# Optimization experiments

Hardware: AMD Instinct MI355X
Metric: run time of the kernel (lower is better)

The kernel has to match this reference:

```python
import jax, jax.numpy as jnp
import numpy as np
from jax import lax

TAU = 2.0          # spikingjelly LIFNode default tau
VTH = 1.0          # v_threshold
ALPHA = 2.0        # ATan surrogate alpha (grad only; fwd is heaviside)
N_WIN = (2, 4, 4)
TOPK = 4
HEADS = 8
EPS = 1e-5


@jax.custom_vjp
def spike(x):
    return (x >= 0).astype(x.dtype)

def _spike_fwd(x):
    return (x >= 0).astype(x.dtype), x

def _spike_bwd(x, g):
    sg = (ALPHA / 2.0) / (1.0 + (jnp.pi / 2.0 * ALPHA * x) ** 2)
    return (g * sg,)

spike.defvjp(_spike_fwd, _spike_bwd)


def lif(x_seq):
    # multi-step LIF, v_reset=None (soft reset), decay_input=True, detach_reset
    def step(v, x):
        v = v + (x - v) / TAU
        s = spike(v - VTH)
        v = v - lax.stop_gradient(s) * VTH
        return v, s
    v0 = jnp.zeros_like(x_seq[0])
    _, s_seq = lax.scan(step, v0, x_seq)
    return s_seq


def bn3d(x, g, b):
    # track_running_stats=False -> always batch stats; step_mode 'm' folds T into batch.
    # x: [T,B,C,Lt,Lh,Lw]; normalize per-channel over (T,B,Lt,Lh,Lw)
    ax = (0, 1, 3, 4, 5)
    m = x.mean(ax, keepdims=True)
    v = x.var(ax, keepdims=True)
    sh = (1, 1, -1, 1, 1, 1)
    return g.reshape(sh) * (x - m) * lax.rsqrt(v + EPS) + b.reshape(sh)


def bra(x, wqkv, bqkv, lepe_w, wo, bo):
    # Bi-level routing attention over 3D windows. x: [N, Lt, Lh, Lw, C]
    N, Lt, Lh, Lw, C = x.shape
    nt, nh, nw = N_WIN
    rt, rh, rw = Lt // nt, Lh // nh, Lw // nw
    R, P = nt * nh * nw, rt * rh * rw
    Dh = C // HEADS

    qkv = x @ wqkv + bqkv                       # [N,Lt,Lh,Lw,3C]
    q, k, v = jnp.split(qkv, 3, axis=-1)

    def to_reg(t):  # -> [N, R, P, C]
        t = t.reshape(N, nt, rt, nh, rh, nw, rw, C)
        return t.transpose(0, 1, 3, 5, 2, 4, 6, 7).reshape(N, R, P, C)

    def from_reg(t):  # [N,R,P,C] -> [N,Lt,Lh,Lw,C]
        t = t.reshape(N, nt, nh, nw, rt, rh, rw, C)
        return t.transpose(0, 1, 4, 2, 5, 3, 6, 7).reshape(N, Lt, Lh, Lw, C)

    qr, kr, vr = to_reg(q), to_reg(k), to_reg(v)

    # coarse routing: region means, top-k region selection
    a_r = jnp.einsum('nrc,nsc->nrs', qr.mean(2), kr.mean(2))   # [N,R,R]
    _, idx = lax.top_k(a_r, TOPK)                               # [N,R,TOPK]

    # gather selected regions' k,v: [N,R,TOPK,P,C] -> [N,R,TOPK*P,H,Dh]
    kg = jax.vmap(lambda a, i: a[i])(kr, idx)
    vg = jax.vmap(lambda a, i: a[i])(vr, idx)
    kg = kg.reshape(N, R, TOPK * P, HEADS, Dh)
    vg = vg.reshape(N, R, TOPK * P, HEADS, Dh)
    qh = qr.reshape(N, R, P, HEADS, Dh)

    logits = jnp.einsum('nrphd,nrkhd->nrhpk', qh * (Dh ** -0.5), kg)
    attn = jax.nn.softmax(logits, axis=-1)
    out = jnp.einsum('nrhpk,nrkhd->nrphd', attn, vg).reshape(N, R, P, C)
    out = from_reg(out)

    # LEPE: depthwise 3x3x3 conv on v
    v_ncdhw = v.transpose(0, 4, 1, 2, 3)
    lepe = lax.conv_general_dilated(
        v_ncdhw, lepe_w, (1, 1, 1), 'SAME', feature_group_count=C,
        dimension_numbers=('NCDHW', 'OIDHW', 'NCDHW'))
    out = out + lepe.transpose(0, 2, 3, 4, 1)

    return out @ wo + bo


def setup_inputs() -> dict:
    key = jax.random.key(0)
    ks = jax.random.split(key, 8)
    T, B, C, Lt, Lh, Lw = 2, 1, 256, 8, 32, 32
    inp = {
        'x': jax.random.normal(ks[0], (T, B, C, Lt, Lh, Lw), jnp.float32),
        'bn1_g': jnp.ones((C,), jnp.float32),
        'bn1_b': jnp.zeros((C,), jnp.float32),
        'wqkv': jax.random.normal(ks[1], (C, 3 * C), jnp.float32) * (C ** -0.5),
        'bqkv': jnp.zeros((3 * C,), jnp.float32),
        'lepe_w': jax.random.normal(ks[2], (C, 1, 3, 3, 3), jnp.float32) * 0.1,
        'wo': jax.random.normal(ks[3], (C, C), jnp.float32) * (C ** -0.5),
        'bo': jnp.zeros((C,), jnp.float32),
        'bn2_g': jnp.ones((C,), jnp.float32),
        'bn2_b': jnp.zeros((C,), jnp.float32),
        'ffn_w1': jax.random.normal(ks[4], (C, 4 * C), jnp.float32) * (C ** -0.5),
        'ffn_b1': jnp.zeros((4 * C,), jnp.float32),
        'ffn_w2': jax.random.normal(ks[5], (4 * C, C), jnp.float32) * ((4 * C) ** -0.5),
        'ffn_b2': jnp.zeros((C,), jnp.float32),
        'scale': jnp.ones((1,), jnp.float32) * 0.5,
    }
    return inp


def reference(x, bn1_g, bn1_b, wqkv, bqkv, lepe_w, wo, bo,
              bn2_g, bn2_b, ffn_w1, ffn_b1, ffn_w2, ffn_b2, scale):
    T, B, C, Lt, Lh, Lw = x.shape

    # --- attention branch ---
    s1 = lif(bn3d(x, bn1_g, bn1_b))                       # [T,B,C,Lt,Lh,Lw]
    sa = s1.transpose(0, 1, 3, 4, 5, 2).reshape(T * B, Lt, Lh, Lw, C)
    a = bra(sa, wqkv, bqkv, lepe_w, wo, bo)
    a = a.reshape(T, B, Lt, Lh, Lw, C).transpose(0, 1, 5, 2, 3, 4)
    x = x + a * scale

    # --- FFN branch (1x1x1 conv = channel GEMM) ---
    s2 = lif(bn3d(x, bn2_g, bn2_b))
    h = jax.nn.gelu(jnp.einsum('tbcdhw,cf->tbfdhw', s2, ffn_w1)
                    + ffn_b1.reshape(1, 1, -1, 1, 1, 1), approximate=False)
    f = (jnp.einsum('tbfdhw,fc->tbcdhw', h, ffn_w2)
         + ffn_b2.reshape(1, 1, -1, 1, 1, 1))
    return x + f * scale
```

## Files before the change

kernel.cpp:

```cpp
#include <hip/hip_runtime.h>
#include <math.h>

#define CC 256
#define LL 8192
#define RR 32
#define PPP 256
#define NTOP 4
#define TOKS 16384
#define TBLK (TOKS * 32)

typedef unsigned short u16;
typedef __attribute__((ext_vector_type(8))) short short8;
typedef __attribute__((ext_vector_type(8))) unsigned short u16x8;
typedef __attribute__((ext_vector_type(4))) float f32x4;
typedef __attribute__((ext_vector_type(4))) unsigned short u16x4;

#if defined(__has_builtin)
#if __has_builtin(__builtin_amdgcn_exp2f)
#define EXP2(x) __builtin_amdgcn_exp2f(x)
#endif
#endif
#ifndef EXP2
#define EXP2(x) exp2f(x)
#endif

__device__ inline u16 f2bf(float f) {
  unsigned int b = __float_as_uint(f);
  unsigned int r = (b + 0x7FFFu + ((b >> 16) & 1u)) >> 16;
  return (u16)r;
}
__device__ inline float bf2f(u16 x) { return __uint_as_float(((unsigned int)x) << 16); }

__global__ __launch_bounds__(256) void k_bnstats(const float* __restrict__ x,
                                                 float* __restrict__ mean,
                                                 float* __restrict__ istd) {
  int c = blockIdx.x, tid = threadIdx.x;
  float s = 0.f, sq = 0.f;
  for (int i = tid; i < 2 * LL / 4; i += 256) {
    int t = i >> 11, l4 = (i & 2047) * 4;
    float4 v = *(const float4*)&x[(size_t)(t * CC + c) * LL + l4];
    s += (v.x + v.y) + (v.z + v.w);
    sq += (v.x * v.x + v.y * v.y) + (v.z * v.z + v.w * v.w);
  }
  __shared__ float rs[256], rq[256];
  rs[tid] = s; rq[tid] = sq;
  __syncthreads();
  for (int off = 128; off > 0; off >>= 1) {
    if (tid < off) { rs[tid] += rs[tid + off]; rq[tid] += rq[tid + off]; }
    __syncthreads();
  }
  if (tid == 0) {
    float m = rs[0] * (1.f / (2 * LL));
    float var = rq[0] * (1.f / (2 * LL)) - m * m;
    mean[c] = m;
    istd[c] = rsqrtf(var + 1e-5f);
  }
}

__global__ __launch_bounds__(128) void k_bnfin(const float* __restrict__ psum,
                                               const float* __restrict__ psq,
                                               float* __restrict__ mean,
                                               float* __restrict__ istd) {
  int c = blockIdx.x;
  int tid = threadIdx.x;
  __shared__ float rs[128], rq[128];
  rs[tid] = psum[c * 128 + tid];
  rq[tid] = psq[c * 128 + tid];
  __syncthreads();
  for (int off = 64; off > 0; off >>= 1) {
    if (tid < off) { rs[tid] += rs[tid + off]; rq[tid] += rq[tid + off]; }
    __syncthreads();
  }
  if (tid == 0) {
    float m = rs[0] * (1.f / 16384.f);
    float var = rq[0] * (1.f / 16384.f) - m * m;
    mean[c] = m;
    istd[c] = rsqrtf(var + 1e-5f);
  }
}

__global__ __launch_bounds__(256) void k_lifT(const float* __restrict__ xin,
                                              const float* __restrict__ mean,
                                              const float* __restrict__ istd,
                                              const float* __restrict__ g,
                                              const float* __restrict__ b,
                                              u16* __restrict__ actT) {
  __shared__ float t0[32][33], t1[32][33];
  int l0 = blockIdx.x * 32, c0 = blockIdx.y * 32;
  int tx = threadIdx.x & 31, ty = threadIdx.x >> 5;
  for (int i = 0; i < 32; i += 8) {
    int c = c0 + ty + i;
    float m = mean[c], is = istd[c], gg = g[c], bb = b[c];
    float x0 = xin[(size_t)c * LL + l0 + tx];
    float x1 = xin[(size_t)(CC + c) * LL + l0 + tx];
    float y0 = gg * (x0 - m) * is + bb;
    float y1 = gg * (x1 - m) * is + bb;
    float v = y0 * 0.5f;
    float s0 = (v >= 1.f) ? 1.f : 0.f;
    v -= s0;
    v += (y1 - v) * 0.5f;
    float s1 = (v >= 1.f) ? 1.f : 0.f;
    t0[ty + i][tx] = s0;
    t1[ty + i][tx] = s1;
  }
  __syncthreads();
  size_t kb = (size_t)(c0 >> 5) * TBLK;
  for (int i = 0; i < 32; i += 8) {
    int l = l0 + ty + i;
    actT[kb + (size_t)l * 32 + tx] = f2bf(t0[tx][ty + i]);
    actT[kb + (size_t)(LL + l) * 32 + tx] = f2bf(t1[tx][ty + i]);
  }
}

__device__ inline void tr_tile(const float* __restrict__ in, u16* __restrict__ out,
                               int C, int c0, int r0) {
  __shared__ float t[32][33];
  int tx = threadIdx.x & 31, ty = threadIdx.x >> 5;
  for (int i = 0; i < 32; i += 8)
    t[ty + i][tx] = in[(size_t)(r0 + ty + i) * C + c0 + tx];
  __syncthreads();
  size_t kb = (size_t)(r0 >> 5) * C * 32;
  for (int i = 0; i < 32; i += 8)
    out[kb + (size_t)(c0 + ty + i) * 32 + tx] = f2bf(t[tx][ty + i]);
}

__global__ __launch_bounds__(256) void k_trall(const float* __restrict__ wqkv,
                                               const float* __restrict__ w1,
                                               const float* __restrict__ w2,
                                               const float* __restrict__ wo,
                                               const float* __restrict__ lep,
                                               u16* __restrict__ wqkvT, u16* __restrict__ w1T,
                                               u16* __restrict__ w2T, u16* __restrict__ woT,
                                               float* __restrict__ wTlep) {
  int b = blockIdx.x;
  if (b < 192) {
    tr_tile(wqkv, wqkvT, 768, (b % 24) * 32, (b / 24) * 32);
  } else if (b < 448) {
    int i = b - 192;
    tr_tile(w1, w1T, 1024, (i % 32) * 32, (i / 32) * 32);
  } else if (b < 704) {
    int i = b - 448;
    tr_tile(w2, w2T, 256, (i % 8) * 32, (i / 8) * 32);
  } else if (b < 768) {
    int i = b - 704;
    tr_tile(wo, woT, 256, (i % 8) * 32, (i / 8) * 32);
  } else {
    int c = threadIdx.x;
    for (int tap = 0; tap < 27; ++tap) wTlep[tap * 256 + c] = lep[c * 27 + tap];
  }
}

template<int MR, int NR, int WCN, int KTOT>
__device__ inline void mfma_core_blk(const u16* __restrict__ A0, int sAb,
                                     const u16* __restrict__ B0, int sBb,
                                     f32x4 acc[MR][NR]) {
  int lane = threadIdx.x & 63;
  int w = threadIdx.x >> 6;
  int wr = w / WCN, wc = w % WCN;
  int u = lane & 15;
  int g8 = (lane >> 4) * 8;
  const u16* Ap = A0 + (wr * MR * 16 + u) * 32 + g8;
  const u16* Bp = B0 + (wc * NR * 16 + u) * 32 + g8;
  constexpr int NKB = KTOT >> 5;
  short8 aA[MR], bA[NR], aB[MR], bB[NR];
#pragma unroll
  for (int i = 0; i < MR; ++i) aA[i] = *(const short8*)(Ap + i * 512);
#pragma unroll
  for (int j = 0; j < NR; ++j) bA[j] = *(const short8*)(Bp + j * 512);
#pragma unroll
  for (int kb = 0; kb < NKB; kb += 2) {
    if (kb + 1 < NKB) {
#pragma unroll
      for (int i = 0; i < MR; ++i) aB[i] = *(const short8*)(Ap + (size_t)(kb + 1) * sAb + i * 512);
#pragma unroll
      for (int j = 0; j < NR; ++j) bB[j] = *(const short8*)(Bp + (size_t)(kb + 1) * sBb + j * 512);
    }
#pragma unroll
    for (int i = 0; i < MR; ++i)
#pragma unroll
      for (int j = 0; j < NR; ++j)
        acc[i][j] = __builtin_amdgcn_mfma_f32_16x16x32_bf16(aA[i], bA[j], acc[i][j], 0, 0, 0);
    if (kb + 2 < NKB) {
#pragma unroll
      for (int i = 0; i < MR; ++i) aA[i] = *(const short8*)(Ap + (size_t)(kb + 2) * sAb + i * 512);
#pragma unroll
      for (int j = 0; j < NR; ++j) bA[j] = *(const short8*)(Bp + (size_t)(kb + 2) * sBb + j * 512);
    }
    if (kb + 1 < NKB) {
#pragma unroll
      for (int i = 0; i < MR; ++i)
#pragma unroll
        for (int j = 0; j < NR; ++j)
          acc[i][j] = __builtin_amdgcn_mfma_f32_16x16x32_bf16(aB[i], bB[j], acc[i][j], 0, 0, 0);
    }
  }
}

__global__ __launch_bounds__(256) void k_gqkv(const u16* __restrict__ spkT, const u16* __restrict__ wT,
                                              const float* __restrict__ bias,
                                              u16* __restrict__ qh, u16* __restrict__ kh,
                                              u16* __restrict__ vt, u16* __restrict__ vtok) {
  f32x4 acc[4][4] = {};
  int m0 = blockIdx.x * 128, n0 = blockIdx.y * 128;
  mfma_core_blk<4, 4, 2, 256>(spkT + (size_t)m0 * 32, TBLK, wT + (size_t)n0 * 32, 768 * 32, acc);
  int lane = threadIdx.x & 63, w = threadIdx.x >> 6;
  int wr = w >> 1, wc = w & 1;
  int u = lane & 15;
  const float QSC = 0.255034865f;
#pragma unroll
  for (int i = 0; i < 4; ++i) {
    int token0 = m0 + wr * 64 + i * 16 + (lane >> 4) * 4;
    int l = token0 & (LL - 1), nb = token0 >> 13;
    int lt = l >> 10, lh = (l >> 5) & 31, lw = l & 31;
    int r = ((lt >> 2) * 4 + (lh >> 3)) * 4 + (lw >> 3);
    int p0 = ((lt & 3) * 8 + (lh & 7)) * 8 + (lw & 7);
    int nr = nb * RR + r;
#pragma unroll
    for (int j = 0; j < 4; ++j) {
      int ch = n0 + wc * 64 + j * 16 + u;
      int which = ch >> 8, c = ch & 255;
      int hh = c >> 5, dh = c & 31;
      size_t hb = ((size_t)nr * 8 + hh) * 8192;
      float bb = bias[ch];
      if (which == 0) {
#pragma unroll
        for (int reg = 0; reg < 4; ++reg)
          qh[hb + (p0 + reg) * 32 + dh] = f2bf((acc[i][j][reg] + bb) * QSC);
      } else if (which == 1) {
#pragma unroll
        for (int reg = 0; reg < 4; ++reg)
          kh[hb + (p0 + reg) * 32 + dh] = f2bf(acc[i][j][reg] + bb);
      } else {
        u16x4 pk;
#pragma unroll
        for (int reg = 0; reg < 4; ++reg) {
          u16 vb = f2bf(acc[i][j][reg] + bb);
          pk[reg] = vb;
          vtok[(size_t)(token0 + reg) * CC + c] = vb;
        }
        *(u16x4*)&vt[hb + dh * 256 + p0] = pk;
      }
    }
  }
}

__global__ __launch_bounds__(256) void k_means(const u16* __restrict__ qh, const u16* __restrict__ kh,
                                               float* __restrict__ qm, float* __restrict__ km) {
  int nrh = blockIdx.x;
  int nr = nrh >> 3, h = nrh & 7;
  int tid = threadIdx.x;
  int dh = tid & 31, pg = tid >> 5;
  size_t base = (size_t)nrh * 8192;
  float sq = 0.f, sk = 0.f;
  for (int p = pg * 32; p < pg * 32 + 32; ++p) {
    sq += bf2f(qh[base + p * 32 + dh]);
    sk += bf2f(kh[base + p * 32 + dh]);
  }
  __shared__ float rq[256], rk[256];
  rq[tid] = sq; rk[tid] = sk;
  __syncthreads();
  if (pg == 0) {
#pragma unroll
    for (int g = 1; g < 8; ++g) { sq += rq[g * 32 + dh]; sk += rk[g * 32 + dh]; }
    qm[nr * 256 + h * 32 + dh] = sq * (1.f / 256);
    km[nr * 256 + h * 32 + dh] = sk * (1.f / 256);
  }
}

__global__ __launch_bounds__(256) void k_route(const float* __restrict__ qm,
                                               const float* __restrict__ km,
                                               int* __restrict__ idx) {
  int nr = blockIdx.x;
  int n = nr >> 5;
  int tid = threadIdx.x;
  int s = tid >> 3, cg = tid & 7;
  const float* qrow = qm + nr * CC;
  const float* krow = km + (n * RR + s) * CC;
  float sum = 0.f;
  for (int c = cg * 32; c < cg * 32 + 32; ++c) sum += qrow[c] * krow[c];
  sum += __shfl_xor(sum, 1);
  sum += __shfl_xor(sum, 2);
  sum += __shfl_xor(sum, 4);
  __shared__ float ar[32];
  if (cg == 0) ar[s] = sum;
  __syncthreads();
  if (tid == 0) {
    for (int t = 0; t < NTOP; ++t) {
      float best = -1e30f; int bi = 0;
      for (int ss = 0; ss < 32; ++ss)
        if (ar[ss] > best) { best = ar[ss]; bi = ss; }
      ar[bi] = -1e30f;
      idx[nr * NTOP + t] = bi;
    }
  }
}

__global__ __launch_bounds__(256) void k_attn_mfma(const u16* __restrict__ qh,
                                                   const u16* __restrict__ kh,
                                                   const u16* __restrict__ vt,
                                                   const int* __restrict__ idx,
                                                   u16* __restrict__ oreg) {
  int h = blockIdx.x, r = blockIdx.y, n = blockIdx.z;
  int nr = n * RR + r;
  int lane = threadIdx.x & 63;
  int w = threadIdx.x >> 6;
  int u = lane & 15, g = lane >> 4;
  int swz = (u >> 1) & 3;
  __shared__ __align__(16) unsigned pl[4096];
  unsigned* plw = &pl[w * 1024];

  const u16* qb = qh + ((size_t)nr * 8 + h) * 8192;
  int q0 = w * 64;
  short8 qf[4];
#pragma unroll
  for (int f = 0; f < 4; ++f)
    qf[f] = *(const short8*)(qb + (size_t)(q0 + f * 16 + u) * 32 + g * 8);

  f32x4 accO[2][4] = {};
  float lsum[4] = {0.f, 0.f, 0.f, 0.f};
  const int* idxp = &idx[nr * NTOP];

  for (int ri = 0; ri < NTOP; ++ri) {
    int reg = idxp[ri];
    size_t rb = ((size_t)(n * RR + reg) * 8 + h) * 8192;
#pragma unroll 2
    for (int t = 0; t < 8; ++t) {
      int pb = t * 32;
      short8 kf0 = *(const short8*)(kh + rb + (size_t)(pb + u) * 32 + g * 8);
      short8 kf1 = *(const short8*)(kh + rb + (size_t)(pb + 16 + u) * 32 + g * 8);
      short8 vf0 = *(const short8*)(vt + rb + (size_t)u * 256 + pb + g * 8);
      short8 vf1 = *(const short8*)(vt + rb + (size_t)(16 + u) * 256 + pb + g * 8);

      f32x4 s0[4], s1[4];
      __builtin_amdgcn_s_setprio(1);
#pragma unroll
      for (int nf = 0; nf < 4; ++nf) {
        s0[nf] = __builtin_amdgcn_mfma_f32_16x16x32_bf16(kf0, qf[nf], (f32x4){0.f, 0.f, 0.f, 0.f}, 0, 0, 0);
        s1[nf] = __builtin_amdgcn_mfma_f32_16x16x32_bf16(kf1, qf[nf], (f32x4){0.f, 0.f, 0.f, 0.f}, 0, 0, 0);
      }
      __builtin_amdgcn_s_setprio(0);
#pragma unroll
      for (int nf = 0; nf < 4; ++nf) {
#pragma unroll
        for (int mf = 0; mf < 2; ++mf) {
          f32x4 sv = mf ? s1[nf] : s0[nf];
          float p0 = EXP2(sv[0]);
          float p1 = EXP2(sv[1]);
          float p2 = EXP2(sv[2]);
          float p3 = EXP2(sv[3]);
          lsum[nf] += (p0 + p1) + (p2 + p3);
          unsigned wA, wB;
          asm("v_cvt_pk_bf16_f32 %0, %1, %2" : "=v"(wA) : "v"(p0), "v"(p1));
          asm("v_cvt_pk_bf16_f32 %0, %1, %2" : "=v"(wB) : "v"(p2), "v"(p3));
          int bidx = (mf * 2 + (g >> 1)) ^ swz;
          *(uint2*)&plw[nf * 256 + u * 16 + bidx * 4 + (g & 1) * 2] = make_uint2(wA, wB);
        }
      }
      __builtin_amdgcn_s_setprio(1);
#pragma unroll
      for (int nf = 0; nf < 4; ++nf) {
        short8 pf = *(const short8*)&plw[nf * 256 + u * 16 + ((g ^ swz) << 2)];
        accO[0][nf] = __builtin_amdgcn_mfma_f32_16x16x32_bf16(vf0, pf, accO[0][nf], 0, 0, 0);
        accO[1][nf] = __builtin_amdgcn_mfma_f32_16x16x32_bf16(vf1, pf, accO[1][nf], 0, 0, 0);
      }
      __builtin_amdgcn_s_setprio(0);
    }
  }

#pragma unroll
  for (int nf = 0; nf < 4; ++nf) {
    lsum[nf] += __shfl_xor(lsum[nf], 16);
    lsum[nf] += __shfl_xor(lsum[nf], 32);
    float inv = 1.f / lsum[nf];
    int q = q0 + nf * 16 + u;
    int z = (((r >> 4) & 1) << 2) | ((q >> 6) & 3);
    int y = (((r >> 2) & 3) << 3) | ((q >> 3) & 7);
    int xx = ((r & 3) << 3) | (q & 7);
    int l = (z << 10) | (y << 5) | xx;
    u16* ob = &oreg[((size_t)(n * LL + l)) * CC + h * 32];
#pragma unroll
    for (int mf = 0; mf < 2; ++mf) {
      f32x4 o = mf ? accO[1][nf] : accO[0][nf];
      float a0 = o[0] * inv, a1 = o[1] * inv, a2 = o[2] * inv, a3 = o[3] * inv;
      unsigned w0, w1;
      asm("v_cvt_pk_bf16_f32 %0, %1, %2" : "=v"(w0) : "v"(a0), "v"(a1));
      asm("v_cvt_pk_bf16_f32 %0, %1, %2" : "=v"(w1) : "v"(a2), "v"(a3));
      *(uint2*)&ob[mf * 16 + g * 4] = make_uint2(w0, w1);
    }
  }
}

__global__ __launch_bounds__(256) void k_lepe(const u16* __restrict__ oreg,
                                              const u16* __restrict__ vtok,
                                              const float* __restrict__ wT,
                                              u16* __restrict__ otok) {
  int vox = threadIdx.x >> 6;
  int b = blockIdx.x * 4 + vox;
  int l = b & (LL - 1);
  int lt = l >> 10, lh = (l >> 5) & 31, lw = l & 31;
  int c4 = (threadIdx.x & 63) * 4;
  const u16* vb = vtok + (size_t)b * CC + c4;
  float lx = 0.f, ly = 0.f, lz = 0.f, lww = 0.f;
#pragma unroll
  for (int dz = -1; dz <= 1; ++dz) {
#pragma unroll
    for (int dy = -1; dy <= 1; ++dy) {
#pragma unroll
      for (int dx = -1; dx <= 1; ++dx) {
        int z = lt + dz, y = lh + dy, xx = lw + dx;
        if (z >= 0 && z < 8 && y >= 0 && y < 32 && xx >= 0 && xx < 32) {
          int tap = ((dz + 1) * 3 + (dy + 1)) * 3 + (dx + 1);
          long off = (long)(dz * 1024 + dy * 32 + dx) * CC;
          float4 w4 = *(const float4*)&wT[tap * 256 + c4];
          u16x4 v4 = *(const u16x4*)&vb[off];
          lx = fmaf(w4.x, bf2f(v4[0]), lx);
          ly = fmaf(w4.y, bf2f(v4[1]), ly);
          lz = fmaf(w4.z, bf2f(v4[2]), lz);
          lww = fmaf(w4.w, bf2f(v4[3]), lww);
        }
      }
    }
  }
  u16x4 a4 = *(const u16x4*)&oreg[(size_t)b * CC + c4];
  size_t oaddr = (size_t)(c4 >> 5) * TBLK + (size_t)b * 32 + (c4 & 31);
  *(u16x4*)&otok[oaddr] =
      (u16x4){f2bf(bf2f(a4[0]) + lx), f2bf(bf2f(a4[1]) + ly),
              f2bf(bf2f(a4[2]) + lz), f2bf(bf2f(a4[3]) + lww)};
}

__global__ __launch_bounds__(256) void k_gffn1(const u16* __restrict__ sT, const u16* __restrict__ wT,
                                               const float* __restrict__ bias, u16* __restrict__ hbuf) {
  __shared__ __align__(16) u16 ot[4 * 128 * 40];
  f32x4 acc[4][4] = {};
  int m0 = blockIdx.x * 128, n0 = blockIdx.y * 128;
  mfma_core_blk<4, 4, 2, 256>(sT + (size_t)m0 * 32, TBLK, wT + (size_t)n0 * 32, 1024 * 32, acc);
  int lane = threadIdx.x & 63, w = threadIdx.x >> 6;
  int wr = w >> 1, wc = w & 1;
  int u = lane & 15, g = lane >> 4;
#pragma unroll
  for (int i = 0; i < 4; ++i) {
#pragma unroll
    for (int reg = 0; reg < 4; ++reg) {
      int tl = wr * 64 + i * 16 + g * 4 + reg;
#pragma unroll
      for (int j = 0; j < 4; ++j) {
        int cl = wc * 64 + j * 16 + u;
        float z = acc[i][j][reg] + bias[n0 + cl];
        float z2 = z * z;
        float ea = z * fmaf(z2, 0.1029431f, 2.3022078f);
        float t = EXP2(ea);
        float th = (t - 1.f) * __builtin_amdgcn_rcpf(t + 1.f);
        float hz = 0.5f * z;
        float gel = fmaf(hz, th, hz);
        ot[(cl >> 5) * (128 * 40) + tl * 40 + (cl & 31)] = f2bf(gel);
      }
    }
  }
  __syncthreads();
  int kb = threadIdx.x >> 6;
  int lt2 = threadIdx.x & 63;
  int tok0 = lt2 >> 2, chunk = lt2 & 3;
  u16* gdst = hbuf + ((size_t)(n0 >> 5) + kb) * TBLK + (size_t)m0 * 32;
  const u16* lsrc = &ot[kb * (128 * 40)];
#pragma unroll
  for (int it = 0; it < 8; ++it) {
    int token = it * 16 + tok0;
    *(u16x8*)(gdst + (size_t)token * 32 + chunk * 8) =
        *(const u16x8*)(lsrc + token * 40 + chunk * 8);
  }
}

__global__ __launch_bounds__(128) void k_gffn2(const u16* __restrict__ w2T, const u16* __restrict__ hb,
                                               const float* __restrict__ bias, const float* __restrict__ scale,
                                               float* __restrict__ out) {
  f32x4 acc[2][4] = {};
  int n0 = blockIdx.x * 128, m0 = blockIdx.y * 32;
  mfma_core_blk<2, 4, 2, 1024>(w2T + (size_t)m0 * 32, 256 * 32, hb + (size_t)n0 * 32, TBLK, acc);
  int lane = threadIdx.x & 63, wc = threadIdx.x >> 6;
  float sc = scale[0];
#pragma unroll
  for (int i = 0; i < 2; ++i) {
#pragma unroll
    for (int reg = 0; reg < 4; ++reg) {
      int ch = m0 + i * 16 + (lane >> 4) * 4 + reg;
      float bb = bias[ch];
#pragma unroll
      for (int j = 0; j < 4; ++j) {
        int token = n0 + wc * 64 + j * 16 + (lane & 15);
        int t = token >> 13, l = token & (LL - 1);
        size_t oi = ((size_t)t * CC + ch) * LL + l;
        out[oi] += (acc[i][j][reg] + bb) * sc;
      }
    }
  }
}

__global__ __launch_bounds__(128) void k_gwo(const u16* __restrict__ woT, const u16* __restrict__ atok,
                                             const float* __restrict__ bias, const float* __restrict__ xin,
                                             const float* __restrict__ scale, float* __restrict__ out,
                                             float* __restrict__ psum, float* __restrict__ psq) {
  f32x4 acc[2][4] = {};
  int n0 = blockIdx.x * 128, m0 = blockIdx.y * 32;
  mfma_core_blk<2, 4, 2, 256>(woT + (size_t)m0 * 32, 256 * 32, atok + (size_t)n0 * 32, TBLK, acc);
  int lane = threadIdx.x & 63, wc = threadIdx.x >> 6;
  int g = lane >> 4;
  float sc = scale[0];
  __shared__ float lsum[2][32], lsq[2][32];
#pragma unroll
  for (int i = 0; i < 2; ++i) {
#pragma unroll
    for (int reg = 0; reg < 4; ++reg) {
      int ch = m0 + i * 16 + g * 4 + reg;
      float bb = bias[ch];
      float s = 0.f, q = 0.f;
#pragma unroll
      for (int j = 0; j < 4; ++j) {
        int token = n0 + wc * 64 + j * 16 + (lane & 15);
        int t = token >> 13, l = token & (LL - 1);
        size_t oi = ((size_t)t * CC + ch) * LL + l;
        float v = xin[oi] + (acc[i][j][reg] + bb) * sc;
        out[oi] = v;
        s += v; q += v * v;
      }
      s += __shfl_xor(s, 1); q += __shfl_xor(q, 1);
      s += __shfl_xor(s, 2); q += __shfl_xor(q, 2);
      s += __shfl_xor(s, 4); q += __shfl_xor(q, 4);
      s += __shfl_xor(s, 8); q += __shfl_xor(q, 8);
      if ((lane & 15) == 0) {
        lsum[wc][i * 16 + g * 4 + reg] = s;
        lsq[wc][i * 16 + g * 4 + reg] = q;
      }
    }
  }
  __syncthreads();
  int tid = threadIdx.x;
  if (tid < 32) {
    psum[(m0 + tid) * 128 + blockIdx.x] = lsum[0][tid] + lsum[1][tid];
    psq[(m0 + tid) * 128 + blockIdx.x] = lsq[0][tid] + lsq[1][tid];
  }
}

extern "C" void kernel_launch(void* const* d_in, const int* in_sizes, int n_in,
                              void* d_out, int out_size, void* d_ws, size_t ws_size,
                              hipStream_t stream) {
  const float* x      = (const float*)d_in[0];
  const float* bn1_g  = (const float*)d_in[1];
  const float* bn1_b  = (const float*)d_in[2];
  const float* wqkv   = (const float*)d_in[3];
  const float* bqkv   = (const float*)d_in[4];
  const float* lepe_w = (const float*)d_in[5];
  const float* wo_w   = (const float*)d_in[6];
  const float* bo     = (const float*)d_in[7];
  const float* bn2_g  = (const float*)d_in[8];
  const float* bn2_b  = (const float*)d_in[9];
  const float* ffn_w1 = (const float*)d_in[10];
  const float* ffn_b1 = (const float*)d_in[11];
  const float* ffn_w2 = (const float*)d_in[12];
  const float* ffn_b2 = (const float*)d_in[13];
  const float* scale  = (const float*)d_in[14];
  float* out = (float*)d_out;

  float* ws    = (float*)d_ws;
  u16*   actT  = (u16*)(ws + 4194304);
  u16*   qhead = (u16*)(ws + 6291456);
  u16*   khead = (u16*)(ws + 8388608);
  u16*   vthead= (u16*)(ws + 10485760);
  u16*   vtok  = (u16*)(ws + 12582912);
  u16*   oreg  = (u16*)(ws + 16777216);
  u16*   hbuf  = (u16*)(ws + 6291456);
  u16*   wqkvT = (u16*)(ws + 20971520);
  u16*   w1T   = (u16*)(ws + 21069824);
  u16*   w2T   = (u16*)(ws + 21200896);
  u16*   woT   = (u16*)(ws + 21331968);
  float* sm    = ws + 21364736;
  float* mean1 = sm;
  float* istd1 = sm + 256;
  float* mean2 = sm + 512;
  float* istd2 = sm + 768;
  float* qm    = sm + 1024;
  float* km    = sm + 1024 + 16384;
  int*   idxb  = (int*)(sm + 1024 + 32768);
  float* wTlep = sm + 1024 + 32768 + 256;
  float* psum  = sm + 1024 + 32768 + 256 + 6912;
  float* psq   = psum + 32768;

  k_trall<<<769, 256, 0, stream>>>(wqkv, ffn_w1, ffn_w2, wo_w, lepe_w,
                                   wqkvT, w1T, w2T, woT, wTlep);

  k_bnstats<<<256, 256, 0, stream>>>(x, mean1, istd1);
  k_lifT<<<dim3(256, 8), 256, 0, stream>>>(x, mean1, istd1, bn1_g, bn1_b, actT);
  k_gqkv<<<dim3(128, 6), 256, 0, stream>>>(actT, wqkvT, bqkv, qhead, khead, vthead, vtok);
  k_means<<<512, 256, 0, stream>>>(qhead, khead, qm, km);
  k_route<<<64, 256, 0, stream>>>(qm, km, idxb);
  k_attn_mfma<<<dim3(8, RR, 2), 256, 0, stream>>>(qhead, khead, vthead, idxb, oreg);
  k_lepe<<<4096, 256, 0, stream>>>(oreg, vtok, wTlep, actT);
  k_gwo<<<dim3(128, 8), 128, 0, stream>>>(woT, actT, bo, x, scale, out, psum, psq);

  k_bnfin<<<256, 128, 0, stream>>>(psum, psq, mean2, istd2);
  k_lifT<<<dim3(256, 8), 256, 0, stream>>>(out, mean2, istd2, bn2_g, bn2_b, actT);
  k_gffn1<<<dim3(128, 8), 256, 0, stream>>>(actT, w1T, ffn_b1, hbuf);
  k_gffn2<<<dim3(128, 8), 128, 0, stream>>>(w2T, hbuf, ffn_b2, scale, out);
}
```

Before: 196.5 us.

## Split K across wave pairs in wo and FFN2 GEMMs with LDS reduction

The k_gwo and k_gffn2 GEMMs go from 128 to 256 threads per block. Each half of the waves handles half of the K dimension, and partial accumulators are reduced through shared memory before the epilogue. The goal is more waves per block for latency hiding and a shorter serial K loop in these small-N GEMMs, which previously ran only two waves per block. The cost is an LDS round trip and a barrier, plus idle upper waves during the epilogue. The MFMA helper is refactored to take explicit wave row and column.

```diff
diff --git a/kernel.cpp b/kernel.cpp
--- a/kernel.cpp
+++ b/kernel.cpp
@@ -150,13 +150,11 @@
   }
 }
 
-template<int MR, int NR, int WCN, int KTOT>
-__device__ inline void mfma_core_blk(const u16* __restrict__ A0, int sAb,
-                                     const u16* __restrict__ B0, int sBb,
-                                     f32x4 acc[MR][NR]) {
+template<int MR, int NR, int KTOT>
+__device__ inline void mfma_core_w(const u16* __restrict__ A0, int sAb,
+                                   const u16* __restrict__ B0, int sBb,
+                                   int wr, int wc, f32x4 acc[MR][NR]) {
   int lane = threadIdx.x & 63;
-  int w = threadIdx.x >> 6;
-  int wr = w / WCN, wc = w % WCN;
   int u = lane & 15;
   int g8 = (lane >> 4) * 8;
   const u16* Ap = A0 + (wr * MR * 16 + u) * 32 + g8;
@@ -202,8 +200,10 @@
                                               u16* __restrict__ vt, u16* __restrict__ vtok) {
   f32x4 acc[4][4] = {};
   int m0 = blockIdx.x * 128, n0 = blockIdx.y * 128;
-  mfma_core_blk<4, 4, 2, 256>(spkT + (size_t)m0 * 32, TBLK, wT + (size_t)n0 * 32, 768 * 32, acc);
-  int lane = threadIdx.x & 63, w = threadIdx.x >> 6;
+  int w = threadIdx.x >> 6;
+  mfma_core_w<4, 4, 256>(spkT + (size_t)m0 * 32, TBLK, wT + (size_t)n0 * 32, 768 * 32,
+                         w >> 1, w & 1, acc);
+  int lane = threadIdx.x & 63;
   int wr = w >> 1, wc = w & 1;
   int u = lane & 15;
   const float QSC = 0.255034865f;
@@ -433,8 +433,10 @@
   __shared__ __align__(16) u16 ot[4 * 128 * 40];
   f32x4 acc[4][4] = {};
   int m0 = blockIdx.x * 128, n0 = blockIdx.y * 128;
-  mfma_core_blk<4, 4, 2, 256>(sT + (size_t)m0 * 32, TBLK, wT + (size_t)n0 * 32, 1024 * 32, acc);
-  int lane = threadIdx.x & 63, w = threadIdx.x >> 6;
+  int w = threadIdx.x >> 6;
+  mfma_core_w<4, 4, 256>(sT + (size_t)m0 * 32, TBLK, wT + (size_t)n0 * 32, 1024 * 32,
+                         w >> 1, w & 1, acc);
+  int lane = threadIdx.x & 63;
   int wr = w >> 1, wc = w & 1;
   int u = lane & 15, g = lane >> 4;
 #pragma unroll
@@ -470,65 +472,103 @@
   }
 }
 
-__global__ __launch_bounds__(128) void k_gffn2(const u16* __restrict__ w2T, const u16* __restrict__ hb,
+__global__ __launch_bounds__(256) void k_gffn2(const u16* __restrict__ w2T, const u16* __restrict__ hb,
                                                const float* __restrict__ bias, const float* __restrict__ scale,
                                                float* __restrict__ out) {
+  __shared__ f32x4 red[2][2][4][64];
   f32x4 acc[2][4] = {};
   int n0 = blockIdx.x * 128, m0 = blockIdx.y * 32;
-  mfma_core_blk<2, 4, 2, 1024>(w2T + (size_t)m0 * 32, 256 * 32, hb + (size_t)n0 * 32, TBLK, acc);
-  int lane = threadIdx.x & 63, wc = threadIdx.x >> 6;
-  float sc = scale[0];
-#pragma unroll
-  for (int i = 0; i < 2; ++i) {
-#pragma unroll
-    for (int reg = 0; reg < 4; ++reg) {
-      int ch = m0 + i * 16 + (lane >> 4) * 4 + reg;
-      float bb = bias[ch];
-#pragma unroll
-      for (int j = 0; j < 4; ++j) {
-        int token = n0 + wc * 64 + j * 16 + (lane & 15);
-        int t = token >> 13, l = token & (LL - 1);
-        size_t oi = ((size_t)t * CC + ch) * LL + l;
-        out[oi] += (acc[i][j][reg] + bb) * sc;
-      }
-    }
-  }
-}
-
-__global__ __launch_bounds__(128) void k_gwo(const u16* __restrict__ woT, const u16* __restrict__ atok,
+  int w = threadIdx.x >> 6, lane = threadIdx.x & 63;
+  int kh2 = w >> 1, wc = w & 1;
+  mfma_core_w<2, 4, 512>(w2T + (size_t)m0 * 32 + (size_t)kh2 * 16 * (256 * 32), 256 * 32,
+                         hb + (size_t)n0 * 32 + (size_t)kh2 * 16 * TBLK, TBLK,
+                         0, wc, acc);
+  if (w >= 2) {
+#pragma unroll
+    for (int i = 0; i < 2; ++i)
+#pragma unroll
+      for (int j = 0; j < 4; ++j)
+        red[w - 2][i][j][lane] = acc[i][j];
+  }
+  __syncthreads();
+  if (w < 2) {
+#pragma unroll
+    for (int i = 0; i < 2; ++i)
+#pragma unroll
+      for (int j = 0; j < 4; ++j)
+        acc[i][j] += red[w][i][j][lane];
+    float sc = scale[0];
+#pragma unroll
+    for (int i = 0; i < 2; ++i) {
+#pragma unroll
+      for (int reg = 0; reg < 4; ++reg) {
+        int ch = m0 + i * 16 + (lane >> 4) * 4 + reg;
+        float bb = bias[ch];
+#pragma unroll
+        for (int j = 0; j < 4; ++j) {
+          int token = n0 + wc * 64 + j * 16 + (lane & 15);
+          int t = token >> 13, l = token & (LL - 1);
+          size_t oi = ((size_t)t * CC + ch) * LL + l;
+          out[oi] += (acc[i][j][reg] + bb) * sc;
+        }
+      }
+    }
+  }
+}
+
+__global__ __launch_bounds__(256) void k_gwo(const u16* __restrict__ woT, const u16* __restrict__ atok,
                                              const float* __restrict__ bias, const float* __restrict__ xin,
                                              const float* __restrict__ scale, float* __restrict__ out,
                                              float* __restrict__ psum, float* __restrict__ psq) {
+  __shared__ f32x4 red[2][2][4][64];
+  __shared__ float lsum[2][32], lsq[2][32];
   f32x4 acc[2][4] = {};
   int n0 = blockIdx.x * 128, m0 = blockIdx.y * 32;
-  mfma_core_blk<2, 4, 2, 256>(woT + (size_t)m0 * 32, 256 * 32, atok + (size_t)n0 * 32, TBLK, acc);
-  int lane = threadIdx.x & 63, wc = threadIdx.x >> 6;
-  int g = lane >> 4;
-  float sc = scale[0];
-  __shared__ float lsum[2][32], lsq[2][32];
-#pragma unroll
-  for (int i = 0; i < 2; ++i) {
-#pragma unroll
-    for (int reg = 0; reg < 4; ++reg) {
-      int ch = m0 + i * 16 + g * 4 + reg;
-      float bb = bias[ch];
-      float s = 0.f, q = 0.f;
-#pragma unroll
-      for (int j = 0; j < 4; ++j) {
-        int token = n0 + wc * 64 + j * 16 + (lane & 15);
-        int t = token >> 13, l = token & (LL - 1);
-        size_t oi = ((size_t)t * CC + ch) * LL + l;
-        float v = xin[oi] + (acc[i][j][reg] + bb) * sc;
-        out[oi] = v;
-        s += v; q += v * v;
-      }
-      s += __shfl_xor(s, 1); q += __shfl_xor(q, 1);
-      s += __shfl_xor(s, 2); q += __shfl_xor(q, 2);
-      s += __shfl_xor(s, 4); q += __shfl_xor(q, 4);
-      s += __shfl_xor(s, 8); q += __shfl_xor(q, 8);
-      if ((lane & 15) == 0) {
-        lsum[wc][i * 16 + g * 4 + reg] = s;
-        lsq[wc][i * 16 + g * 4 + reg] = q;
+  int w = threadIdx.x >> 6, lane = threadIdx.x & 63;
+  int kh2 = w >> 1, wc = w & 1;
+  mfma_core_w<2, 4, 128>(woT + (size_t)m0 * 32 + (size_t)kh2 * 4 * (256 * 32), 256 * 32,
+                         atok + (size_t)n0 * 32 + (size_t)kh2 * 4 * TBLK, TBLK,
+                         0, wc, acc);
+  if (w >= 2) {
+#pragma unroll
+    for (int i = 0; i < 2; ++i)
+#pragma unroll
+      for (int j = 0; j < 4; ++j)
+        red[w - 2][i][j][lane] = acc[i][j];
+  }
+  __syncthreads();
+  if (w < 2) {
+    int g = lane >> 4;
+    float sc = scale[0];
+#pragma unroll
+    for (int i = 0; i < 2; ++i)
+#pragma unroll
+      for (int j = 0; j < 4; ++j)
+        acc[i][j] += red[w][i][j][lane];
+#pragma unroll
+    for (int i = 0; i < 2; ++i) {
+#pragma unroll
+      for (int reg = 0; reg < 4; ++reg) {
+        int ch = m0 + i * 16 + g * 4 + reg;
+        float bb = bias[ch];
+        float s = 0.f, q = 0.f;
+#pragma unroll
+        for (int j = 0; j < 4; ++j) {
+          int token = n0 + wc * 64 + j * 16 + (lane & 15);
+          int t = token >> 13, l = token & (LL - 1);
+          size_t oi = ((size_t)t * CC + ch) * LL + l;
+          float v = xin[oi] + (acc[i][j][reg] + bb) * sc;
+          out[oi] = v;
+          s += v; q += v * v;
+        }
+        s += __shfl_xor(s, 1); q += __shfl_xor(q, 1);
+        s += __shfl_xor(s, 2); q += __shfl_xor(q, 2);
+        s += __shfl_xor(s, 4); q += __shfl_xor(q, 4);
+        s += __shfl_xor(s, 8); q += __shfl_xor(q, 8);
+        if ((lane & 15) == 0) {
+          lsum[wc][i * 16 + g * 4 + reg] = s;
+          lsq[wc][i * 16 + g * 4 + reg] = q;
+        }
       }
     }
   }
@@ -594,10 +634,10 @@
   k_route<<<64, 256, 0, stream>>>(qm, km, idxb);
   k_attn_mfma<<<dim3(8, RR, 2), 256, 0, stream>>>(qhead, khead, vthead, idxb, oreg);
   k_lepe<<<4096, 256, 0, stream>>>(oreg, vtok, wTlep, actT);
-  k_gwo<<<dim3(128, 8), 128, 0, stream>>>(woT, actT, bo, x, scale, out, psum, psq);
+  k_gwo<<<dim3(128, 8), 256, 0, stream>>>(woT, actT, bo, x, scale, out, psum, psq);
 
   k_bnfin<<<256, 128, 0, stream>>>(psum, psq, mean2, istd2);
   k_lifT<<<dim3(256, 8), 256, 0, stream>>>(out, mean2, istd2, bn2_g, bn2_b, actT);
   k_gffn1<<<dim3(128, 8), 256, 0, stream>>>(actT, w1T, ffn_b1, hbuf);
-  k_gffn2<<<dim3(128, 8), 128, 0, stream>>>(w2T, hbuf, ffn_b2, scale, out);
-}
+  k_gffn2<<<dim3(128, 8), 256, 0, stream>>>(w2T, hbuf, ffn_b2, scale, out);
+}
```

Result: no change. 195.4 us (-0.6%).
